# Performance work log

Measured on AMD Instinct MI355X. Metric: run time of the kernel, lower is better.

The kernel has to match this reference:

```python
import jax, jax.numpy as jnp
import numpy as np

# pywt db4 decomposition filters (dec_lo, dec_hi), 8 taps
DEC_LO = np.array([-0.010597401784997278, 0.032883011666982945, 0.030841381835986965,
                   -0.18703481171888114, -0.02798376941698385, 0.6308807679295904,
                   0.7148465705525415, 0.23037781330885523], dtype=np.float32)
DEC_HI = np.array([-0.23037781330885523, 0.7148465705525415, -0.6308807679295904,
                   -0.02798376941698385, 0.18703481171888114, 0.030841381835986965,
                   -0.032883011666982945, -0.010597401784997278], dtype=np.float32)
FLEN = 8
LEVELS = 5


def _dwt_level(x):
    """Single-level DWT matching pywt.dwt(x, 'db4', mode='symmetric').

    x: [N, L] -> (cA, cD) each [N, (L + FLEN - 1) // 2]
    Equivalent to: ext = symmetric pad by FLEN-1 each side;
    np.convolve(ext, filt, 'valid')[1::2].
    """
    ext = jnp.pad(x, ((0, 0), (FLEN - 1, FLEN - 1)), mode='symmetric')
    ext = ext[:, 1:]  # offset so stride-2 hits full-conv positions 1,3,5,...
    # true convolution == lax cross-correlation with reversed filter
    k = jnp.stack([jnp.asarray(DEC_LO, x.dtype)[::-1],
                   jnp.asarray(DEC_HI, x.dtype)[::-1]])[:, None, :]  # [2,1,F]
    y = jax.lax.conv_general_dilated(ext[:, None, :], k,
                                     window_strides=(2,), padding='VALID')
    return y[:, 0, :], y[:, 1, :]


def setup_inputs() -> dict:
    key = jax.random.key(0)
    x = jax.random.normal(key, (64, 64, 4096), dtype=jnp.float32)
    return {"x": x}


def reference(x):
    B, C, T = x.shape
    a = x.reshape(B * C, T)
    details = []  # cD1, cD2, ..., cD5 (finest first)
    for _ in range(LEVELS):
        a, d = _dwt_level(a)
        details.append(d)
    approx = a.reshape(B, C, -1)
    # module returns details ordered coarsest-first: [cD5, cD4, ..., cD1]
    detail_coeffs = [d.reshape(B, C, -1) for d in details[::-1]]
    return (approx, *detail_coeffs)
```

## Files before the change

### kernel.cpp

```cpp
#include <hip/hip_runtime.h>

#define T0 4096
#define NLEV 5
#define BLOCK 256

__constant__ float c_LO[8] = {
    -0.010597401784997278f, 0.032883011666982945f, 0.030841381835986965f,
    -0.18703481171888114f, -0.02798376941698385f, 0.6308807679295904f,
    0.7148465705525415f, 0.23037781330885523f};
__constant__ float c_HI[8] = {
    -0.23037781330885523f, 0.7148465705525415f, -0.6308807679295904f,
    -0.02798376941698385f, 0.18703481171888114f, 0.030841381835986965f,
    -0.032883011666982945f, -0.010597401784997278f};

__device__ __forceinline__ int symidx(int t, int L) {
    t = (t < 0) ? (-1 - t) : t;
    t = (t >= L) ? (2 * L - 1 - t) : t;
    return t;
}

__global__ __launch_bounds__(BLOCK) void dwt5_kernel(
    const float* __restrict__ x, float* __restrict__ out,
    long long offA, long long offD1, long long offD2, long long offD3,
    long long offD4, long long offD5)
{
    __shared__ float bufA[T0];
    __shared__ float bufB[2051 + 1];

    const int row = blockIdx.x;
    const int tid = threadIdx.x;
    const float* __restrict__ xrow = x + (size_t)row * T0;

    for (int j = tid; j < T0 / 4; j += BLOCK) {
        float4 v = reinterpret_cast<const float4*>(xrow)[j];
        bufA[4 * j + 0] = v.x;
        bufA[4 * j + 1] = v.y;
        bufA[4 * j + 2] = v.z;
        bufA[4 * j + 3] = v.w;
    }
    __syncthreads();

    long long dOff[NLEV] = {offD1, offD2, offD3, offD4, offD5};

    float* src = bufA;
    float* dst = bufB;
    int L = T0;
    for (int lev = 0; lev < NLEV; ++lev) {
        const int nOut = (L + 7) >> 1;
        float* __restrict__ dSeg = out + dOff[lev] + (long long)row * nOut;
        float* __restrict__ aSeg = out + offA + (long long)row * nOut;
        for (int i = tid; i < nOut; i += BLOCK) {
            const int base = 2 * i + 1;
            float lo = 0.f, hi = 0.f;
#pragma unroll
            for (int m = 0; m < 8; ++m) {
                const float v = src[symidx(base - m, L)];
                lo = fmaf(c_LO[m], v, lo);
                hi = fmaf(c_HI[m], v, hi);
            }
            dSeg[i] = hi;
            if (lev == NLEV - 1) {
                aSeg[i] = lo;
            } else {
                dst[i] = lo;
            }
        }
        __syncthreads();
        float* tmp = src; src = dst; dst = tmp;
        L = nOut;
    }
}

extern "C" void kernel_launch(void* const* d_in, const int* in_sizes, int n_in,
                              void* d_out, int out_size, void* d_ws, size_t ws_size,
                              hipStream_t stream) {
    const float* x = (const float*)d_in[0];
    float* out = (float*)d_out;

    const int rows = in_sizes[0] / T0;
    const int n1 = (T0 + 7) / 2;
    const int n2 = (n1 + 7) / 2;
    const int n3 = (n2 + 7) / 2;
    const int n4 = (n3 + 7) / 2;
    const int n5 = (n4 + 7) / 2;

    const long long offA  = 0;
    const long long offD5 = offA  + (long long)rows * n5;
    const long long offD4 = offD5 + (long long)rows * n5;
    const long long offD3 = offD4 + (long long)rows * n4;
    const long long offD2 = offD3 + (long long)rows * n3;
    const long long offD1 = offD2 + (long long)rows * n2;

    dwt5_kernel<<<rows, BLOCK, 0, stream>>>(x, out, offA, offD1, offD2, offD3,
                                            offD4, offD5);
}
```

Baseline: 129.2 us.

## Store pre-padded symmetric extensions in LDS and read taps as float2

Each level's signal is now kept in shared memory with its symmetric border already written out: the edge mirrors are filled while loading and while writing each level's output. This removes the per-tap symidx branching, so the eight taps can be read as four aligned float2 loads. Filter coefficients become compile-time immediates instead of constant-memory loads, and the global output writes use nontemporal stores. The cost is extra conditional border writes and slightly larger LDS buffers, and correctness depends on getting the pad offsets right at every level.

```diff
diff --git a/kernel.cpp b/kernel.cpp
--- a/kernel.cpp
+++ b/kernel.cpp
@@ -3,29 +3,33 @@
 #define T0 4096
 #define NLEV 5
 #define BLOCK 256
+#define PAD 6
 
-__constant__ float c_LO[8] = {
-    -0.010597401784997278f, 0.032883011666982945f, 0.030841381835986965f,
-    -0.18703481171888114f, -0.02798376941698385f, 0.6308807679295904f,
-    0.7148465705525415f, 0.23037781330885523f};
-__constant__ float c_HI[8] = {
-    -0.23037781330885523f, 0.7148465705525415f, -0.6308807679295904f,
-    -0.02798376941698385f, 0.18703481171888114f, 0.030841381835986965f,
-    -0.032883011666982945f, -0.010597401784997278f};
+#define RLO0  0.23037781330885523f
+#define RLO1  0.7148465705525415f
+#define RLO2  0.6308807679295904f
+#define RLO3 -0.02798376941698385f
+#define RLO4 -0.18703481171888114f
+#define RLO5  0.030841381835986965f
+#define RLO6  0.032883011666982945f
+#define RLO7 -0.010597401784997278f
 
-__device__ __forceinline__ int symidx(int t, int L) {
-    t = (t < 0) ? (-1 - t) : t;
-    t = (t >= L) ? (2 * L - 1 - t) : t;
-    return t;
-}
+#define RHI0 -0.010597401784997278f
+#define RHI1 -0.032883011666982945f
+#define RHI2  0.030841381835986965f
+#define RHI3  0.18703481171888114f
+#define RHI4 -0.02798376941698385f
+#define RHI5 -0.6308807679295904f
+#define RHI6  0.7148465705525415f
+#define RHI7 -0.23037781330885523f
 
 __global__ __launch_bounds__(BLOCK) void dwt5_kernel(
     const float* __restrict__ x, float* __restrict__ out,
     long long offA, long long offD1, long long offD2, long long offD3,
     long long offD4, long long offD5)
 {
-    __shared__ float bufA[T0];
-    __shared__ float bufB[2051 + 1];
+    __shared__ float extA[T0 + 16];
+    __shared__ float extB[2051 + 16];
 
     const int row = blockIdx.x;
     const int tid = threadIdx.x;
@@ -33,36 +37,63 @@
 
     for (int j = tid; j < T0 / 4; j += BLOCK) {
         float4 v = reinterpret_cast<const float4*>(xrow)[j];
-        bufA[4 * j + 0] = v.x;
-        bufA[4 * j + 1] = v.y;
-        bufA[4 * j + 2] = v.z;
-        bufA[4 * j + 3] = v.w;
+        const int b = 4 * j;
+        float w[4] = {v.x, v.y, v.z, v.w};
+        extA[PAD + b + 0] = w[0];
+        extA[PAD + b + 1] = w[1];
+        extA[PAD + b + 2] = w[2];
+        extA[PAD + b + 3] = w[3];
+        if (b < 8) {
+#pragma unroll
+            for (int k = 0; k < 4; ++k) {
+                const int s = b + k;
+                if (s < 6) extA[5 - s] = w[k];
+            }
+        }
+        if (b >= T0 - 8) {
+#pragma unroll
+            for (int k = 0; k < 4; ++k) {
+                const int s = b + k;
+                if (s >= T0 - 7) extA[PAD + T0 + (T0 - 1 - s)] = w[k];
+            }
+        }
     }
     __syncthreads();
 
-    long long dOff[NLEV] = {offD1, offD2, offD3, offD4, offD5};
+    const long long dOff[NLEV] = {offD1, offD2, offD3, offD4, offD5};
 
-    float* src = bufA;
-    float* dst = bufB;
+    float* src = extA;
+    float* dst = extB;
     int L = T0;
+#pragma unroll
     for (int lev = 0; lev < NLEV; ++lev) {
         const int nOut = (L + 7) >> 1;
         float* __restrict__ dSeg = out + dOff[lev] + (long long)row * nOut;
         float* __restrict__ aSeg = out + offA + (long long)row * nOut;
+        const float2* __restrict__ e2 = reinterpret_cast<const float2*>(src);
         for (int i = tid; i < nOut; i += BLOCK) {
-            const int base = 2 * i + 1;
-            float lo = 0.f, hi = 0.f;
-#pragma unroll
-            for (int m = 0; m < 8; ++m) {
-                const float v = src[symidx(base - m, L)];
-                lo = fmaf(c_LO[m], v, lo);
-                hi = fmaf(c_HI[m], v, hi);
-            }
-            dSeg[i] = hi;
+            const float2 w0 = e2[i + 0];
+            const float2 w1 = e2[i + 1];
+            const float2 w2 = e2[i + 2];
+            const float2 w3 = e2[i + 3];
+
+            float lo, hi;
+            lo = RLO0 * w0.x;            hi = RHI0 * w0.x;
+            lo = fmaf(RLO1, w0.y, lo);   hi = fmaf(RHI1, w0.y, hi);
+            lo = fmaf(RLO2, w1.x, lo);   hi = fmaf(RHI2, w1.x, hi);
+            lo = fmaf(RLO3, w1.y, lo);   hi = fmaf(RHI3, w1.y, hi);
+            lo = fmaf(RLO4, w2.x, lo);   hi = fmaf(RHI4, w2.x, hi);
+            lo = fmaf(RLO5, w2.y, lo);   hi = fmaf(RHI5, w2.y, hi);
+            lo = fmaf(RLO6, w3.x, lo);   hi = fmaf(RHI6, w3.x, hi);
+            lo = fmaf(RLO7, w3.y, lo);   hi = fmaf(RHI7, w3.y, hi);
+
+            __builtin_nontemporal_store(hi, &dSeg[i]);
             if (lev == NLEV - 1) {
-                aSeg[i] = lo;
+                __builtin_nontemporal_store(lo, &aSeg[i]);
             } else {
-                dst[i] = lo;
+                dst[PAD + i] = lo;
+                if (i < 6)          dst[5 - i] = lo;
+                if (i >= nOut - 7)  dst[PAD + nOut + (nOut - 1 - i)] = lo;
             }
         }
         __syncthreads();
```

After: 113.8 us. -11.9%, faster.
